# Kernel optimization log

Hardware: AMD Instinct MI355X
Metric: run time of the kernel (lower is better)

The kernel has to match this reference:

```python
import jax, jax.numpy as jnp
import numpy as np

DIM = 768
NUM_HEADS = 12
HEAD_DIM = DIM // NUM_HEADS
SCALE = HEAD_DIM ** -0.5


def setup_inputs() -> dict:
    key = jax.random.key(0)
    k_x, k_qkv, k_proj, k_pb = jax.random.split(key, 4)
    B, N, C = 16, 1024, DIM
    x = jax.random.normal(k_x, (B, N, C), dtype=jnp.float32)
    # qkv Linear: weight [3C, C], no bias (qkv_bias=False)
    w_qkv = jax.random.normal(k_qkv, (3 * C, C), dtype=jnp.float32) * (C ** -0.5)
    # proj Linear: weight [C, C], bias [C]
    w_proj = jax.random.normal(k_proj, (C, C), dtype=jnp.float32) * (C ** -0.5)
    b_proj = jax.random.normal(k_pb, (C,), dtype=jnp.float32) * 0.01
    return {"x": x, "w_qkv": w_qkv, "w_proj": w_proj, "b_proj": b_proj}


def reference(x, w_qkv, w_proj, b_proj):
    B, N, C = x.shape
    H, D = NUM_HEADS, HEAD_DIM
    # qkv projection: [B,N,3C] -> [3,B,H,N,D]
    qkv = jnp.einsum('bnc,ec->bne', x, w_qkv)
    qkv = qkv.reshape(B, N, 3, H, D).transpose(2, 0, 3, 1, 4)
    q, k, v = qkv[0], qkv[1], qkv[2]
    # manual attention: scores [B,H,N,N] materialized, as in source
    attn = jnp.einsum('bhqd,bhkd->bhqk', q, k) * SCALE
    attn = jax.nn.softmax(attn, axis=-1)
    out = jnp.einsum('bhqk,bhkd->bhqd', attn, v)  # [B,H,N,D]
    out = out.transpose(0, 2, 1, 3).reshape(B, N, C)
    out = jnp.einsum('bnc,oc->bno', out, w_proj) + b_proj
    return out
```

## Files before the change

### kernel.cpp

```cpp
#include <hip/hip_runtime.h>
#include <hip/hip_bf16.h>
#include <stdint.h>

typedef __attribute__((ext_vector_type(8))) short short8;
typedef __attribute__((ext_vector_type(4))) short short4v;
typedef __attribute__((ext_vector_type(4))) float floatx4;

#define B_   16
#define N_   1024
#define C_   768
#define H_   12
#define D_   64
#define K_   768
#define QSCALE 0.18033688011112042f

__device__ __forceinline__ short f2bf(float f) {
    __hip_bfloat16 h = __float2bfloat16(f);
    short s; __builtin_memcpy(&s, &h, 2); return s;
}

__device__ __forceinline__ short8 ld8_f32(const float* p) {
    float4 u = *(const float4*)p;
    float4 v = *(const float4*)(p + 4);
    short8 r;
    r[0] = f2bf(u.x); r[1] = f2bf(u.y); r[2] = f2bf(u.z); r[3] = f2bf(u.w);
    r[4] = f2bf(v.x); r[5] = f2bf(v.y); r[6] = f2bf(v.z); r[7] = f2bf(v.w);
    return r;
}

template<int MODE>
__global__ __launch_bounds__(256, 2)
void gemm_bt(const void* __restrict__ Ap, const float* __restrict__ Bm,
             const float* __restrict__ bias,
             short* __restrict__ q_ws, short* __restrict__ k_ws,
             short* __restrict__ v_ws, float* __restrict__ outp)
{
    __shared__ short Alds[128 * 32];
    __shared__ short Blds[128 * 32];
    const int tid  = threadIdx.x;
    const int wave = tid >> 6, lane = tid & 63;
    const int cl   = lane & 15, quad = lane >> 4;
    const int bm = blockIdx.x, bn = blockIdx.y;
    const int wm = (wave >> 1) * 64, wn = (wave & 1) * 64;

    const long Abase = (long)bm * 128 * K_;
    const long Bbase = (long)bn * 128 * K_;
    const int srow = tid >> 2;
    const int scol = (tid & 3) * 8;

    const floatx4 fzero = {0.f, 0.f, 0.f, 0.f};
    floatx4 acc[4][4];
    #pragma unroll
    for (int i = 0; i < 4; i++)
        #pragma unroll
        for (int j = 0; j < 4; j++) acc[i][j] = fzero;

    for (int kt = 0; kt < K_; kt += 32) {
        short8 a0, a1;
        if (MODE == 0) {
            const float* Af = (const float*)Ap;
            a0 = ld8_f32(Af + Abase + (long)srow * K_ + kt + scol);
            a1 = ld8_f32(Af + Abase + (long)(srow + 64) * K_ + kt + scol);
        } else {
            const short* As = (const short*)Ap;
            a0 = *(const short8*)(As + Abase + (long)srow * K_ + kt + scol);
            a1 = *(const short8*)(As + Abase + (long)(srow + 64) * K_ + kt + scol);
        }
        short8 b0 = ld8_f32(Bm + Bbase + (long)srow * K_ + kt + scol);
        short8 b1 = ld8_f32(Bm + Bbase + (long)(srow + 64) * K_ + kt + scol);
        __syncthreads();
        *(short8*)(Alds + srow * 32 + scol)        = a0;
        *(short8*)(Alds + (srow + 64) * 32 + scol) = a1;
        *(short8*)(Blds + srow * 32 + scol)        = b0;
        *(short8*)(Blds + (srow + 64) * 32 + scol) = b1;
        __syncthreads();

        short8 af[4], bf[4];
        #pragma unroll
        for (int i = 0; i < 4; i++)
            af[i] = *(const short8*)(Alds + (wm + i * 16 + cl) * 32 + quad * 8);
        #pragma unroll
        for (int j = 0; j < 4; j++)
            bf[j] = *(const short8*)(Blds + (wn + j * 16 + cl) * 32 + quad * 8);
        #pragma unroll
        for (int i = 0; i < 4; i++)
            #pragma unroll
            for (int j = 0; j < 4; j++)
                acc[i][j] = __builtin_amdgcn_mfma_f32_16x16x32_bf16(af[i], bf[j], acc[i][j], 0, 0, 0);
    }

    #pragma unroll
    for (int i = 0; i < 4; i++) {
        const int gm0 = bm * 128 + wm + i * 16 + quad * 4;
        #pragma unroll
        for (int j = 0; j < 4; j++) {
            const int gn = bn * 128 + wn + j * 16 + cl;
            if (MODE == 0) {
                const int t   = bn / 6;
                const int rem = gn - t * 768;
                const int h   = rem >> 6, d = rem & 63;
                const int b   = gm0 >> 10;
                const int n0  = gm0 & 1023;
                const int bh  = b * H_ + h;
                if (t == 2) {
                    short4v pk;
                    #pragma unroll
                    for (int r = 0; r < 4; r++) pk[r] = f2bf(acc[i][j][r]);
                    *(short4v*)(v_ws + (((long)(bh * D_ + d)) << 10) + n0) = pk;
                } else {
                    short* dst = (t == 0) ? q_ws : k_ws;
                    const float sc = (t == 0) ? QSCALE : 1.0f;
                    #pragma unroll
                    for (int r = 0; r < 4; r++)
                        dst[((long)bh * N_ + (n0 + r)) * D_ + d] = f2bf(acc[i][j][r] * sc);
                }
            } else {
                const float bv = bias[gn];
                #pragma unroll
                for (int r = 0; r < 4; r++)
                    outp[(long)(gm0 + r) * C_ + gn] = acc[i][j][r] + bv;
            }
        }
    }
}

__global__ __launch_bounds__(256, 2)
void attn_fused(const short* __restrict__ q_ws, const short* __restrict__ k_ws,
                const short* __restrict__ v_ws, short* __restrict__ o_ws)
{
    __shared__ short Klds[128 * 72];
    __shared__ short Vlds[64 * 136];
    __shared__ short Plds[4][16 * 136];

    const int tid  = threadIdx.x;
    const int wave = tid >> 6, lane = tid & 63;
    const int cl   = lane & 15, quad = lane >> 4;
    const int qt = blockIdx.x, bh = blockIdx.y;

    const long base = (long)bh * (N_ * D_);
    const int qrow = qt * 64 + wave * 16 + cl;

    const short8 qf0 = *(const short8*)(q_ws + base + (long)qrow * D_ + quad * 8);
    const short8 qf1 = *(const short8*)(q_ws + base + (long)qrow * D_ + 32 + quad * 8);

    const floatx4 fzero = {0.f, 0.f, 0.f, 0.f};
    float m_r[4], l_r[4];
    floatx4 o_acc[4];
    #pragma unroll
    for (int r = 0; r < 4; r++) { m_r[r] = -1e30f; l_r[r] = 0.f; }
    #pragma unroll
    for (int dt = 0; dt < 4; dt++) o_acc[dt] = fzero;

    const int skey = tid >> 3, sseg = (tid & 7) * 8;
    const int vd   = tid >> 4, vseg = (tid & 15) * 8;
    short* pl = &Plds[wave][0];

    for (int kc = 0; kc < N_; kc += 128) {
        short8 kst[4], vst[4];
        #pragma unroll
        for (int p = 0; p < 4; p++) {
            kst[p] = *(const short8*)(k_ws + base + (long)(kc + p * 32 + skey) * D_ + sseg);
            vst[p] = *(const short8*)(v_ws + base + (long)(p * 16 + vd) * N_ + kc + vseg);
        }
        __syncthreads();
        #pragma unroll
        for (int p = 0; p < 4; p++) {
            *(short8*)(Klds + (p * 32 + skey) * 72 + sseg)  = kst[p];
            *(short8*)(Vlds + (p * 16 + vd) * 136 + vseg)   = vst[p];
        }
        __syncthreads();

        floatx4 s[8];
        #pragma unroll
        for (int nt = 0; nt < 8; nt++) {
            short8 kf0 = *(const short8*)(Klds + (nt * 16 + cl) * 72 + quad * 8);
            short8 kf1 = *(const short8*)(Klds + (nt * 16 + cl) * 72 + 32 + quad * 8);
            floatx4 t4 = fzero;
            t4 = __builtin_amdgcn_mfma_f32_16x16x32_bf16(qf0, kf0, t4, 0, 0, 0);
            t4 = __builtin_amdgcn_mfma_f32_16x16x32_bf16(qf1, kf1, t4, 0, 0, 0);
            s[nt] = t4;
        }

        float alpha[4];
        #pragma unroll
        for (int r = 0; r < 4; r++) {
            float v = s[0][r];
            #pragma unroll
            for (int nt = 1; nt < 8; nt++) v = fmaxf(v, s[nt][r]);
            v = fmaxf(v, __shfl_xor(v, 1));
            v = fmaxf(v, __shfl_xor(v, 2));
            v = fmaxf(v, __shfl_xor(v, 4));
            v = fmaxf(v, __shfl_xor(v, 8));
            const float mn = fmaxf(m_r[r], v);
            alpha[r] = __builtin_amdgcn_exp2f(m_r[r] - mn);
            m_r[r] = mn;
            l_r[r] *= alpha[r];
        }
        #pragma unroll
        for (int nt = 0; nt < 8; nt++) {
            #pragma unroll
            for (int r = 0; r < 4; r++) {
                const float p = __builtin_amdgcn_exp2f(s[nt][r] - m_r[r]);
                l_r[r] += p;
                pl[(quad * 4 + r) * 136 + nt * 16 + cl] = f2bf(p);
            }
        }
        #pragma unroll
        for (int dt = 0; dt < 4; dt++) {
            o_acc[dt][0] *= alpha[0]; o_acc[dt][1] *= alpha[1];
            o_acc[dt][2] *= alpha[2]; o_acc[dt][3] *= alpha[3];
        }
        asm volatile("" ::: "memory");

        #pragma unroll
        for (int ks = 0; ks < 4; ks++) {
            short8 pf = *(const short8*)(pl + cl * 136 + ks * 32 + quad * 8);
            #pragma unroll
            for (int dt = 0; dt < 4; dt++) {
                short8 vf = *(const short8*)(Vlds + (dt * 16 + cl) * 136 + ks * 32 + quad * 8);
                o_acc[dt] = __builtin_amdgcn_mfma_f32_16x16x32_bf16(pf, vf, o_acc[dt], 0, 0, 0);
            }
        }
        asm volatile("" ::: "memory");
    }

    #pragma unroll
    for (int r = 0; r < 4; r++) {
        float v = l_r[r];
        v += __shfl_xor(v, 1); v += __shfl_xor(v, 2);
        v += __shfl_xor(v, 4); v += __shfl_xor(v, 8);
        l_r[r] = 1.0f / v;
    }
    const int b = bh / H_, h = bh - b * H_;
    const int nrow = qt * 64 + wave * 16 + quad * 4;
    #pragma unroll
    for (int dt = 0; dt < 4; dt++) {
        const int c = h * D_ + dt * 16 + cl;
        #pragma unroll
        for (int r = 0; r < 4; r++)
            o_ws[((long)(b * N_ + nrow + r)) * C_ + c] = f2bf(o_acc[dt][r] * l_r[r]);
    }
}

extern "C" void kernel_launch(void* const* d_in, const int* in_sizes, int n_in,
                              void* d_out, int out_size, void* d_ws, size_t ws_size,
                              hipStream_t stream)
{
    const float* x      = (const float*)d_in[0];
    const float* w_qkv  = (const float*)d_in[1];
    const float* w_proj = (const float*)d_in[2];
    const float* b_proj = (const float*)d_in[3];
    float* out = (float*)d_out;

    const long SZ = (long)B_ * N_ * C_;
    short* q_ws = (short*)d_ws;
    short* k_ws = q_ws + SZ;
    short* v_ws = k_ws + SZ;
    short* o_ws = v_ws + SZ;

    gemm_bt<0><<<dim3(128, 18), 256, 0, stream>>>(x, w_qkv, nullptr, q_ws, k_ws, v_ws, nullptr);
    attn_fused<<<dim3(16, 192), 256, 0, stream>>>(q_ws, k_ws, v_ws, o_ws);
    gemm_bt<1><<<dim3(128, 6), 256, 0, stream>>>(o_ws, w_proj, b_proj, nullptr, nullptr, nullptr, out);
}
```

Before: 371.3 us.

## Pre-convert inputs to bf16, use direct global-to-LDS loads, enlarge attention tiles

New measurement: 321.6 us. 1.15x faster.

```diff
diff --git a/kernel.cpp b/kernel.cpp
--- a/kernel.cpp
+++ b/kernel.cpp
@@ -19,18 +19,27 @@
     short s; __builtin_memcpy(&s, &h, 2); return s;
 }
 
-__device__ __forceinline__ short8 ld8_f32(const float* p) {
-    float4 u = *(const float4*)p;
-    float4 v = *(const float4*)(p + 4);
+__device__ __forceinline__ void gl_lds16(const void* g, void* l) {
+    __builtin_amdgcn_global_load_lds(
+        (const __attribute__((address_space(1))) unsigned int*)g,
+        (__attribute__((address_space(3))) unsigned int*)l, 16, 0, 0);
+}
+
+__global__ void cvt_bf16(const float* __restrict__ in, short* __restrict__ out, int n8)
+{
+    const int i = blockIdx.x * 256 + threadIdx.x;
+    if (i >= n8) return;
+    const float4* p = (const float4*)in + 2 * (long)i;
+    const float4 u = p[0], v = p[1];
     short8 r;
     r[0] = f2bf(u.x); r[1] = f2bf(u.y); r[2] = f2bf(u.z); r[3] = f2bf(u.w);
     r[4] = f2bf(v.x); r[5] = f2bf(v.y); r[6] = f2bf(v.z); r[7] = f2bf(v.w);
-    return r;
+    *((short8*)out + i) = r;
 }
 
 template<int MODE>
 __global__ __launch_bounds__(256, 2)
-void gemm_bt(const void* __restrict__ Ap, const float* __restrict__ Bm,
+void gemm_bt(const short* __restrict__ A, const short* __restrict__ Bm,
              const float* __restrict__ bias,
              short* __restrict__ q_ws, short* __restrict__ k_ws,
              short* __restrict__ v_ws, float* __restrict__ outp)
@@ -43,10 +52,10 @@
     const int bm = blockIdx.x, bn = blockIdx.y;
     const int wm = (wave >> 1) * 64, wn = (wave & 1) * 64;
 
-    const long Abase = (long)bm * 128 * K_;
-    const long Bbase = (long)bn * 128 * K_;
-    const int srow = tid >> 2;
-    const int scol = (tid & 3) * 8;
+    const short* Ag = A  + (long)bm * 128 * K_ + (long)(tid >> 2) * K_ + (tid & 3) * 8;
+    const short* Bg = Bm + (long)bn * 128 * K_ + (long)(tid >> 2) * K_ + (tid & 3) * 8;
+    short* la = Alds + (tid & 0xC0) * 8;
+    short* lb = Blds + (tid & 0xC0) * 8;
 
     const floatx4 fzero = {0.f, 0.f, 0.f, 0.f};
     floatx4 acc[4][4];
@@ -56,23 +65,11 @@
         for (int j = 0; j < 4; j++) acc[i][j] = fzero;
 
     for (int kt = 0; kt < K_; kt += 32) {
-        short8 a0, a1;
-        if (MODE == 0) {
-            const float* Af = (const float*)Ap;
-            a0 = ld8_f32(Af + Abase + (long)srow * K_ + kt + scol);
-            a1 = ld8_f32(Af + Abase + (long)(srow + 64) * K_ + kt + scol);
-        } else {
-            const short* As = (const short*)Ap;
-            a0 = *(const short8*)(As + Abase + (long)srow * K_ + kt + scol);
-            a1 = *(const short8*)(As + Abase + (long)(srow + 64) * K_ + kt + scol);
-        }
-        short8 b0 = ld8_f32(Bm + Bbase + (long)srow * K_ + kt + scol);
-        short8 b1 = ld8_f32(Bm + Bbase + (long)(srow + 64) * K_ + kt + scol);
-        __syncthreads();
-        *(short8*)(Alds + srow * 32 + scol)        = a0;
-        *(short8*)(Alds + (srow + 64) * 32 + scol) = a1;
-        *(short8*)(Blds + srow * 32 + scol)        = b0;
-        *(short8*)(Blds + (srow + 64) * 32 + scol) = b1;
+        __syncthreads();
+        gl_lds16(Ag + kt,            la);
+        gl_lds16(Ag + kt + 64 * K_,  la + 2048);
+        gl_lds16(Bg + kt,            lb);
+        gl_lds16(Bg + kt + 64 * K_,  lb + 2048);
         __syncthreads();
 
         short8 af[4], bf[4];
@@ -135,21 +132,31 @@
     const int tid  = threadIdx.x;
     const int wave = tid >> 6, lane = tid & 63;
     const int cl   = lane & 15, quad = lane >> 4;
-    const int qt = blockIdx.x, bh = blockIdx.y;
+
+    const int linear = blockIdx.y * 8 + blockIdx.x;
+    const int xcd = linear & 7, slot = linear >> 3;
+    const int bh  = xcd * 24 + (slot >> 3);
+    const int qt  = slot & 7;
 
     const long base = (long)bh * (N_ * D_);
-    const int qrow = qt * 64 + wave * 16 + cl;
-
-    const short8 qf0 = *(const short8*)(q_ws + base + (long)qrow * D_ + quad * 8);
-    const short8 qf1 = *(const short8*)(q_ws + base + (long)qrow * D_ + 32 + quad * 8);
+    const int  qr0  = qt * 128 + wave * 32 + cl;
+
+    short8 qf[2][2];
+    #pragma unroll
+    for (int mt = 0; mt < 2; mt++) {
+        qf[mt][0] = *(const short8*)(q_ws + base + (long)(qr0 + mt * 16) * D_ + quad * 8);
+        qf[mt][1] = *(const short8*)(q_ws + base + (long)(qr0 + mt * 16) * D_ + 32 + quad * 8);
+    }
 
     const floatx4 fzero = {0.f, 0.f, 0.f, 0.f};
-    float m_r[4], l_r[4];
-    floatx4 o_acc[4];
-    #pragma unroll
-    for (int r = 0; r < 4; r++) { m_r[r] = -1e30f; l_r[r] = 0.f; }
-    #pragma unroll
-    for (int dt = 0; dt < 4; dt++) o_acc[dt] = fzero;
+    float m_r[2][4], l_r[2][4];
+    floatx4 o_acc[2][4];
+    #pragma unroll
+    for (int mt = 0; mt < 2; mt++)
+        #pragma unroll
+        for (int r = 0; r < 4; r++) {
+            m_r[mt][r] = -1e30f; l_r[mt][r] = 0.f; o_acc[mt][r] = fzero;
+        }
 
     const int skey = tid >> 3, sseg = (tid & 7) * 8;
     const int vd   = tid >> 4, vseg = (tid & 15) * 8;
@@ -165,80 +172,86 @@
         __syncthreads();
         #pragma unroll
         for (int p = 0; p < 4; p++) {
-            *(short8*)(Klds + (p * 32 + skey) * 72 + sseg)  = kst[p];
-            *(short8*)(Vlds + (p * 16 + vd) * 136 + vseg)   = vst[p];
-        }
-        __syncthreads();
-
-        floatx4 s[8];
-        #pragma unroll
-        for (int nt = 0; nt < 8; nt++) {
-            short8 kf0 = *(const short8*)(Klds + (nt * 16 + cl) * 72 + quad * 8);
-            short8 kf1 = *(const short8*)(Klds + (nt * 16 + cl) * 72 + 32 + quad * 8);
-            floatx4 t4 = fzero;
-            t4 = __builtin_amdgcn_mfma_f32_16x16x32_bf16(qf0, kf0, t4, 0, 0, 0);
-            t4 = __builtin_amdgcn_mfma_f32_16x16x32_bf16(qf1, kf1, t4, 0, 0, 0);
-            s[nt] = t4;
-        }
-
-        float alpha[4];
+            *(short8*)(Klds + (p * 32 + skey) * 72 + sseg) = kst[p];
+            *(short8*)(Vlds + (p * 16 + vd) * 136 + vseg)  = vst[p];
+        }
+        __syncthreads();
+
+        #pragma unroll
+        for (int mt = 0; mt < 2; mt++) {
+            floatx4 s[8];
+            #pragma unroll
+            for (int nt = 0; nt < 8; nt++) {
+                short8 kf0 = *(const short8*)(Klds + (nt * 16 + cl) * 72 + quad * 8);
+                short8 kf1 = *(const short8*)(Klds + (nt * 16 + cl) * 72 + 32 + quad * 8);
+                floatx4 t4 = fzero;
+                t4 = __builtin_amdgcn_mfma_f32_16x16x32_bf16(qf[mt][0], kf0, t4, 0, 0, 0);
+                t4 = __builtin_amdgcn_mfma_f32_16x16x32_bf16(qf[mt][1], kf1, t4, 0, 0, 0);
+                s[nt] = t4;
+            }
+
+            float alpha[4];
+            #pragma unroll
+            for (int r = 0; r < 4; r++) {
+                float v = s[0][r];
+                #pragma unroll
+                for (int nt = 1; nt < 8; nt++) v = fmaxf(v, s[nt][r]);
+                v = fmaxf(v, __shfl_xor(v, 1));
+                v = fmaxf(v, __shfl_xor(v, 2));
+                v = fmaxf(v, __shfl_xor(v, 4));
+                v = fmaxf(v, __shfl_xor(v, 8));
+                const float mn = fmaxf(m_r[mt][r], v);
+                alpha[r] = __builtin_amdgcn_exp2f(m_r[mt][r] - mn);
+                m_r[mt][r] = mn;
+                l_r[mt][r] *= alpha[r];
+            }
+            #pragma unroll
+            for (int nt = 0; nt < 8; nt++) {
+                #pragma unroll
+                for (int r = 0; r < 4; r++) {
+                    const float p = __builtin_amdgcn_exp2f(s[nt][r] - m_r[mt][r]);
+                    l_r[mt][r] += p;
+                    pl[(quad * 4 + r) * 136 + nt * 16 + cl] = f2bf(p);
+                }
+            }
+            #pragma unroll
+            for (int dt = 0; dt < 4; dt++) {
+                o_acc[mt][dt][0] *= alpha[0]; o_acc[mt][dt][1] *= alpha[1];
+                o_acc[mt][dt][2] *= alpha[2]; o_acc[mt][dt][3] *= alpha[3];
+            }
+            asm volatile("" ::: "memory");
+
+            #pragma unroll
+            for (int ks = 0; ks < 4; ks++) {
+                short8 pf = *(const short8*)(pl + cl * 136 + ks * 32 + quad * 8);
+                #pragma unroll
+                for (int dt = 0; dt < 4; dt++) {
+                    short8 vf = *(const short8*)(Vlds + (dt * 16 + cl) * 136 + ks * 32 + quad * 8);
+                    o_acc[mt][dt] = __builtin_amdgcn_mfma_f32_16x16x32_bf16(pf, vf, o_acc[mt][dt], 0, 0, 0);
+                }
+            }
+            asm volatile("" ::: "memory");
+        }
+    }
+
+    const int b = bh / H_, h = bh - b * H_;
+    #pragma unroll
+    for (int mt = 0; mt < 2; mt++) {
         #pragma unroll
         for (int r = 0; r < 4; r++) {
-            float v = s[0][r];
-            #pragma unroll
-            for (int nt = 1; nt < 8; nt++) v = fmaxf(v, s[nt][r]);
-            v = fmaxf(v, __shfl_xor(v, 1));
-            v = fmaxf(v, __shfl_xor(v, 2));
-            v = fmaxf(v, __shfl_xor(v, 4));
-            v = fmaxf(v, __shfl_xor(v, 8));
-            const float mn = fmaxf(m_r[r], v);
-            alpha[r] = __builtin_amdgcn_exp2f(m_r[r] - mn);
-            m_r[r] = mn;
-            l_r[r] *= alpha[r];
-        }
-        #pragma unroll
-        for (int nt = 0; nt < 8; nt++) {
-            #pragma unroll
-            for (int r = 0; r < 4; r++) {
-                const float p = __builtin_amdgcn_exp2f(s[nt][r] - m_r[r]);
-                l_r[r] += p;
-                pl[(quad * 4 + r) * 136 + nt * 16 + cl] = f2bf(p);
-            }
-        }
+            float v = l_r[mt][r];
+            v += __shfl_xor(v, 1); v += __shfl_xor(v, 2);
+            v += __shfl_xor(v, 4); v += __shfl_xor(v, 8);
+            l_r[mt][r] = 1.0f / v;
+        }
+        const int nrow = qt * 128 + wave * 32 + mt * 16 + quad * 4;
         #pragma unroll
         for (int dt = 0; dt < 4; dt++) {
-            o_acc[dt][0] *= alpha[0]; o_acc[dt][1] *= alpha[1];
-            o_acc[dt][2] *= alpha[2]; o_acc[dt][3] *= alpha[3];
-        }
-        asm volatile("" ::: "memory");
-
-        #pragma unroll
-        for (int ks = 0; ks < 4; ks++) {
-            short8 pf = *(const short8*)(pl + cl * 136 + ks * 32 + quad * 8);
-            #pragma unroll
-            for (int dt = 0; dt < 4; dt++) {
-                short8 vf = *(const short8*)(Vlds + (dt * 16 + cl) * 136 + ks * 32 + quad * 8);
-                o_acc[dt] = __builtin_amdgcn_mfma_f32_16x16x32_bf16(pf, vf, o_acc[dt], 0, 0, 0);
-            }
-        }
-        asm volatile("" ::: "memory");
-    }
-
-    #pragma unroll
-    for (int r = 0; r < 4; r++) {
-        float v = l_r[r];
-        v += __shfl_xor(v, 1); v += __shfl_xor(v, 2);
-        v += __shfl_xor(v, 4); v += __shfl_xor(v, 8);
-        l_r[r] = 1.0f / v;
-    }
-    const int b = bh / H_, h = bh - b * H_;
-    const int nrow = qt * 64 + wave * 16 + quad * 4;
-    #pragma unroll
-    for (int dt = 0; dt < 4; dt++) {
-        const int c = h * D_ + dt * 16 + cl;
-        #pragma unroll
-        for (int r = 0; r < 4; r++)
-            o_ws[((long)(b * N_ + nrow + r)) * C_ + c] = f2bf(o_acc[dt][r] * l_r[r]);
+            const int c = h * D_ + dt * 16 + cl;
+            #pragma unroll
+            for (int r = 0; r < 4; r++)
+                o_ws[((long)(b * N_ + nrow + r)) * C_ + c] = f2bf(o_acc[mt][dt][r] * l_r[mt][r]);
+        }
     }
 }
 
@@ -253,12 +266,19 @@
     float* out = (float*)d_out;
 
     const long SZ = (long)B_ * N_ * C_;
-    short* q_ws = (short*)d_ws;
-    short* k_ws = q_ws + SZ;
-    short* v_ws = k_ws + SZ;
-    short* o_ws = v_ws + SZ;
-
-    gemm_bt<0><<<dim3(128, 18), 256, 0, stream>>>(x, w_qkv, nullptr, q_ws, k_ws, v_ws, nullptr);
-    attn_fused<<<dim3(16, 192), 256, 0, stream>>>(q_ws, k_ws, v_ws, o_ws);
-    gemm_bt<1><<<dim3(128, 6), 256, 0, stream>>>(o_ws, w_proj, b_proj, nullptr, nullptr, nullptr, out);
-}
+    short* q_ws   = (short*)d_ws;
+    short* k_ws   = q_ws + SZ;
+    short* v_ws   = k_ws + SZ;
+    short* x_bf   = v_ws + SZ;
+    short* o_ws   = x_bf;
+    short* wqkv_bf  = x_bf + SZ;
+    short* wproj_bf = wqkv_bf + (long)3 * C_ * C_;
+
+    cvt_bf16<<<dim3(6144), 256, 0, stream>>>(x,      x_bf,     (int)(SZ / 8));
+    cvt_bf16<<<dim3(864),  256, 0, stream>>>(w_qkv,  wqkv_bf,  3 * C_ * C_ / 8);
+    cvt_bf16<<<dim3(288),  256, 0, stream>>>(w_proj, wproj_bf, C_ * C_ / 8);
+
+    gemm_bt<0><<<dim3(128, 18), 256, 0, stream>>>(x_bf, wqkv_bf, nullptr, q_ws, k_ws, v_ws, nullptr);
+    attn_fused<<<dim3(8, 192), 256, 0, stream>>>(q_ws, k_ws, v_ws, o_ws);
+    gemm_bt<1><<<dim3(128, 6), 256, 0, stream>>>(o_ws, wproj_bf, b_proj, nullptr, nullptr, nullptr, out);
+}
```
